# Optimization experiments

Measured on AMD Instinct MI355X. Metric: run time of the kernel, lower is better.

## Reference

```python
import jax, jax.numpy as jnp
import numpy as np
from jax import lax

PH = PW = 7  # patch size


def _unfold2d(x, ph, pw):
    # x: [B, C, H, W] -> patches [B*Ho*Wo, C*ph*pw], channel-major like F.unfold
    B, C, H, W = x.shape
    patches = lax.conv_general_dilated_patches(
        x, filter_shape=(ph, pw), window_strides=(1, 1), padding='VALID')
    # patches: [B, C*ph*pw, Ho, Wo] with feature order (c, i, j) matching F.unfold
    Ho, Wo = H - ph + 1, W - pw + 1
    D = C * ph * pw
    q2d = patches.reshape(B, D, Ho * Wo).transpose(0, 2, 1).reshape(B * Ho * Wo, D)
    return q2d, (B, C, H, W, Ho, Wo, D)


def _fold2d_mean(res, shape_info):
    # res: [B*Ho*Wo, D] patch values -> overlap-add mean image [B, C, H, W]
    B, C, H, W, Ho, Wo, D = shape_info
    res = res.reshape(B, Ho, Wo, C, PH, PW)
    out = jnp.zeros((B, C, H, W), dtype=res.dtype)
    cnt = jnp.zeros((H, W), dtype=res.dtype)
    for di in range(PH):          # small fixed 7x7 loop over patch offsets
        for dj in range(PW):
            out = out.at[:, :, di:di + Ho, dj:dj + Wo].add(
                res[:, :, :, :, di, dj].transpose(0, 3, 1, 2))
            cnt = cnt.at[di:di + Ho, dj:dj + Wo].add(1.0)
    return out / cnt  # reduce='mean'


def setup_inputs() -> dict:
    key = jax.random.key(0)
    k1, k2, k3 = jax.random.split(key, 3)
    query = jax.random.normal(k1, (1, 3, 96, 96), dtype=jnp.float32)
    kmat = jax.random.normal(k2, (8100, 147), dtype=jnp.float32)
    vmat = jax.random.normal(k3, (8100, 147), dtype=jnp.float32)
    return {"query": query, "key": kmat, "value": vmat}


def reference(query, key, value):
    # 1) unfold query image into patch rows [Nq, D]
    q2d, shape_info = _unfold2d(query, PH, PW)
    # 2) nearest-neighbor lookup: squared-euclidean argmin over key rows
    qn = jnp.sum(q2d * q2d, axis=1, keepdims=True)        # [Nq, 1]
    kn = jnp.sum(key * key, axis=1)                       # [Nk]
    dist = qn + kn[None, :] - 2.0 * (q2d @ key.T)         # [Nq, Nk]
    idx = jnp.argmin(dist, axis=1)                        # [Nq]
    # 3) gather matched value patches and fold back (overlap-add mean)
    res = value[idx]                                      # [Nq, D]
    return _fold2d_mean(res, shape_info)
```

## Files before the change

kernel.cpp:

```cpp
#include <hip/hip_runtime.h>


#define NQ 8100
#define NK 8100
#define DD 147
#define HO 90
#define IMG 96
#define NCH 5
#define CST 262144
#define ARRN (NCH * CST)

typedef _Float16 half8 __attribute__((ext_vector_type(8)));
typedef float f32x4 __attribute__((ext_vector_type(4)));

__device__ __forceinline__ void gld16(const _Float16* g, _Float16* l) {
    __builtin_amdgcn_global_load_lds(
        (const __attribute__((address_space(1))) unsigned int*)g,
        (__attribute__((address_space(3))) unsigned int*)l, 16, 0, 0);
}

__global__ void k_prep(const float* __restrict__ query, const float* __restrict__ key,
                       _Float16* __restrict__ Qh, _Float16* __restrict__ Ql,
                       _Float16* __restrict__ Kh, _Float16* __restrict__ Kl,
                       float* __restrict__ kn, unsigned long long* __restrict__ fidx64) {
    const int bx = blockIdx.x;
    const bool isK = (blockIdx.y != 0);

    if (bx >= 640) {
        if (!isK) return;
        int wave = threadIdx.x >> 6, lane = threadIdx.x & 63;
        int kb = ((bx - 640) * 4 + wave) * 16;
        for (int r = 0; r < 16; ++r) {
            int k = kb + r;
            float s = 0.f;
            if (k < NK)
                for (int d = lane; d < DD; d += 64) {
                    float v = key[k * DD + d];
                    s += v * v;
                }
#pragma unroll
            for (int off = 32; off; off >>= 1) s += __shfl_down(s, off, 64);
            if (lane == 0) {
                kn[k] = (k < NK) ? s : 1e30f;
                fidx64[k] = 0xFFFFFFFFFFFFFFFFull;
            }
        }
        return;
    }

    int t = bx * 256 + threadIdx.x;
    int c = t >> 15;
    int rem = t & 32767;
    int col = ((rem >> 6) << 4) + (rem & 15);
    int quad = (rem >> 4) & 3;
    int kbase = c * 32 + quad * 8;

    float v[8];
#pragma unroll
    for (int j = 0; j < 8; ++j) {
        int k = kbase + j;
        float x = 0.f;
        if (k < DD && col < NQ) {
            if (isK) {
                x = key[col * DD + k];
            } else {
                int c3 = k / 49, r2 = k - 49 * c3;
                int rr = r2 / 7, ss = r2 - 7 * rr;
                int y = col / HO, xx = col - HO * y;
                x = query[(c3 * IMG + y + rr) * IMG + xx + ss];
            }
        }
        v[j] = x;
    }
    half8 h8, l8;
#pragma unroll
    for (int j = 0; j < 8; ++j) {
        _Float16 h = (_Float16)v[j];
        h8[j] = h;
        l8[j] = (_Float16)((v[j] - (float)h) * 2048.0f);
    }
    if (isK) {
        *(half8*)(Kh + t * 8) = h8;
        *(half8*)(Kl + t * 8) = l8;
    } else {
        *(half8*)(Qh + t * 8) = h8;
        *(half8*)(Ql + t * 8) = l8;
    }
}

__launch_bounds__(256, 2)
__global__ void k_nn(const _Float16* __restrict__ Qh, const _Float16* __restrict__ Ql,
                     const _Float16* __restrict__ Kh, const _Float16* __restrict__ Kl,
                     const float* __restrict__ kn, unsigned long long* __restrict__ out) {
    __shared__ __align__(16) char smem[65536];
    _Float16* sbase = (_Float16*)smem;

    const int tid = (int)threadIdx.x;
    const int wave = tid >> 6, lane = tid & 63;
    const int l15 = lane & 15, quad = lane >> 4;

    const int b = (int)blockIdx.x;
    const int xcd = b & 7;
    const int i = b >> 3;
    const int qt = (xcd >> 1) * 16 + (i & 15);
    const int kt = (xcd & 1) * 32 + (i >> 4);

    const int mbase = (wave >> 1) * 64;
    const int nbase = (wave & 1) * 64;
    const int q0 = qt * 128, n0 = kt * 128;

    const _Float16* gsrc = (wave == 0) ? Qh : (wave == 1) ? Ql : (wave == 2) ? Kh : Kl;
    const int gbase = ((wave < 2) ? qt : kt) * 8;
    const _Float16* gp0 = gsrc + gbase * 512 + lane * 8;
    _Float16* ldst0 = sbase + wave * 4096 + lane * 8;

    f32x4 acc0[4][4], acc1[4][4];
#pragma unroll
    for (int ii = 0; ii < 4; ++ii)
#pragma unroll
        for (int j = 0; j < 4; ++j) {
            acc0[ii][j] = (f32x4)0.f;
            acc1[ii][j] = (f32x4)0.f;
        }

    const int agrp = (mbase >> 4);
    const int bgrp = (nbase >> 4);

#pragma unroll
    for (int grp = 0; grp < 8; ++grp)
        gld16(gp0 + grp * 512, ldst0 + grp * 512);

#pragma unroll
    for (int c = 0; c < NCH; ++c) {
        __syncthreads();
        if (c + 1 < NCH) {
            const _Float16* gp = gp0 + (c + 1) * CST;
            _Float16* ld = ldst0 + ((c + 1) & 1) * 16384;
#pragma unroll
            for (int grp = 0; grp < 8; ++grp)
                gld16(gp + grp * 512, ld + grp * 512);
        }

        const _Float16* sQh = sbase + (c & 1) * 16384;
        const _Float16* sQl = sQh + 4096;
        const _Float16* sKh = sQh + 8192;
        const _Float16* sKl = sQh + 12288;

        half8 ah[4], al[4];
#pragma unroll
        for (int mt = 0; mt < 4; ++mt) {
            int aoff = (agrp + mt) * 512 + lane * 8;
            ah[mt] = *(const half8*)(sQh + aoff);
            al[mt] = *(const half8*)(sQl + aoff);
        }
#pragma unroll
        for (int nt = 0; nt < 4; ++nt) {
            int boff = (bgrp + nt) * 512 + lane * 8;
            half8 bh = *(const half8*)(sKh + boff);
            half8 bl = *(const half8*)(sKl + boff);
#pragma unroll
            for (int mt = 0; mt < 4; ++mt) {
                acc0[mt][nt] = __builtin_amdgcn_mfma_f32_16x16x32_f16(ah[mt], bh, acc0[mt][nt], 0, 0, 0);
                acc1[mt][nt] = __builtin_amdgcn_mfma_f32_16x16x32_f16(ah[mt], bl, acc1[mt][nt], 0, 0, 0);
                acc1[mt][nt] = __builtin_amdgcn_mfma_f32_16x16x32_f16(al[mt], bh, acc1[mt][nt], 0, 0, 0);
            }
        }
    }

    float knv[4];
    int nglob[4];
#pragma unroll
    for (int nt = 0; nt < 4; ++nt) {
        nglob[nt] = n0 + nbase + nt * 16 + l15;
        knv[nt] = kn[nglob[nt]];
    }
    __syncthreads();
    float* redv = (float*)smem;
    int* redi = (int*)(smem + 17408);

#pragma unroll
    for (int mt = 0; mt < 4; ++mt)
#pragma unroll
        for (int r = 0; r < 4; ++r) {
            float bv = 1e38f;
            int bn = 0x7fffffff;
#pragma unroll
            for (int nt = 0; nt < 4; ++nt) {
                float d = knv[nt] - 2.0f * (acc0[mt][nt][r] + acc1[mt][nt][r] * (1.0f / 2048.0f));
                if (d < bv) { bv = d; bn = nglob[nt]; }
            }
            int m = mbase + mt * 16 + quad * 4 + r;
            int cidx = (nbase >> 2) + l15;
            redv[m * 33 + cidx] = bv;
            redi[m * 33 + cidx] = bn;
        }
    __syncthreads();

    if (tid < 128) {
        float bv = 1e38f;
        int bn = 0x7fffffff;
        for (int t2 = 0; t2 < 32; ++t2) {
            float v = redv[tid * 33 + t2];
            int n = redi[tid * 33 + t2];
            if (v < bv || (v == bv && n < bn)) { bv = v; bn = n; }
        }
        unsigned u = __float_as_uint(bv);
        u = (u & 0x80000000u) ? ~u : (u | 0x80000000u);
        unsigned long long pk = ((unsigned long long)u << 32) | (unsigned)bn;
        atomicMin(&out[q0 + tid], pk);
    }
}

__global__ void k_fold(const float* __restrict__ value,
                       const unsigned long long* __restrict__ fidx64,
                       float* __restrict__ out) {
    int t = blockIdx.x * 256 + threadIdx.x;
    if (t >= 3 * IMG * IMG) return;
    int c = t / (IMG * IMG);
    int rem = t % (IMG * IMG);
    int Y = rem / IMG, X = rem % IMG;
    int i0 = max(0, Y - (HO - 1)), i1 = min(6, Y);
    int j0 = max(0, X - (HO - 1)), j1 = min(6, X);
    float s = 0.f;
    for (int i = i0; i <= i1; ++i)
        for (int j = j0; j <= j1; ++j) {
            int p = (Y - i) * HO + (X - j);
            int row = (int)(fidx64[p] & 0xFFFFFFFFull);
            s += value[row * DD + c * 49 + i * 7 + j];
        }
    float cnt = (float)((i1 - i0 + 1) * (j1 - j0 + 1));
    out[t] = s / cnt;
}

extern "C" void kernel_launch(void* const* d_in, const int* in_sizes, int n_in,
                              void* d_out, int out_size, void* d_ws, size_t ws_size,
                              hipStream_t stream) {
    const float* query = (const float*)d_in[0];
    const float* key   = (const float*)d_in[1];
    const float* value = (const float*)d_in[2];
    float* out = (float*)d_out;

    _Float16* Qh = (_Float16*)d_ws;
    _Float16* Ql = Qh + ARRN;
    _Float16* Kh = Ql + ARRN;
    _Float16* Kl = Kh + ARRN;
    float* kn = (float*)(Kl + ARRN);
    unsigned long long* fidx64 = (unsigned long long*)(kn + 8192);

    dim3 gp(768, 2);
    k_prep<<<gp, 256, 0, stream>>>(query, key, Qh, Ql, Kh, Kl, kn, fidx64);
    k_nn<<<4096, 256, 0, stream>>>(Qh, Ql, Kh, Kl, kn, fidx64);
    k_fold<<<108, 256, 0, stream>>>(value, fidx64, out);
}
```

Before: 164.1 us.

## Keep query fragments in registers and loop over eight key tiles per block

The nearest-neighbour kernel now loads each block's query tile once into registers for all K-chunks. It then iterates over eight key tiles, reading key fragments straight from global memory instead of staging them through LDS with async loads. A running argmin is kept per query, so each block issues one atomicMin per query instead of one per key tile, and the grid shrinks from 4096 to 512 blocks. This trades LDS staging and double buffering for direct global loads and much higher register pressure (80 half8 query registers plus 32 accumulators), which may reduce occupancy. With 512 blocks there may also be too little parallelism to hide memory latency.

```diff
diff --git a/kernel.cpp b/kernel.cpp
--- a/kernel.cpp
+++ b/kernel.cpp
@@ -12,12 +12,6 @@
 
 typedef _Float16 half8 __attribute__((ext_vector_type(8)));
 typedef float f32x4 __attribute__((ext_vector_type(4)));
-
-__device__ __forceinline__ void gld16(const _Float16* g, _Float16* l) {
-    __builtin_amdgcn_global_load_lds(
-        (const __attribute__((address_space(1))) unsigned int*)g,
-        (__attribute__((address_space(3))) unsigned int*)l, 16, 0, 0);
-}
 
 __global__ void k_prep(const float* __restrict__ query, const float* __restrict__ key,
                        _Float16* __restrict__ Qh, _Float16* __restrict__ Ql,
@@ -92,121 +86,104 @@
 __global__ void k_nn(const _Float16* __restrict__ Qh, const _Float16* __restrict__ Ql,
                      const _Float16* __restrict__ Kh, const _Float16* __restrict__ Kl,
                      const float* __restrict__ kn, unsigned long long* __restrict__ out) {
-    __shared__ __align__(16) char smem[65536];
-    _Float16* sbase = (_Float16*)smem;
+    __shared__ float redv[128 * 33];
+    __shared__ int   redi[128 * 33];
 
     const int tid = (int)threadIdx.x;
     const int wave = tid >> 6, lane = tid & 63;
     const int l15 = lane & 15, quad = lane >> 4;
+    const int mbase = (wave >> 1) * 64;
+    const int nbase = (wave & 1) * 64;
 
     const int b = (int)blockIdx.x;
     const int xcd = b & 7;
-    const int i = b >> 3;
-    const int qt = (xcd >> 1) * 16 + (i & 15);
-    const int kt = (xcd & 1) * 32 + (i >> 4);
-
-    const int mbase = (wave >> 1) * 64;
-    const int nbase = (wave & 1) * 64;
-    const int q0 = qt * 128, n0 = kt * 128;
-
-    const _Float16* gsrc = (wave == 0) ? Qh : (wave == 1) ? Ql : (wave == 2) ? Kh : Kl;
-    const int gbase = ((wave < 2) ? qt : kt) * 8;
-    const _Float16* gp0 = gsrc + gbase * 512 + lane * 8;
-    _Float16* ldst0 = sbase + wave * 4096 + lane * 8;
-
-    f32x4 acc0[4][4], acc1[4][4];
-#pragma unroll
-    for (int ii = 0; ii < 4; ++ii)
-#pragma unroll
-        for (int j = 0; j < 4; ++j) {
-            acc0[ii][j] = (f32x4)0.f;
-            acc1[ii][j] = (f32x4)0.f;
-        }
-
-    const int agrp = (mbase >> 4);
-    const int bgrp = (nbase >> 4);
-
-#pragma unroll
-    for (int grp = 0; grp < 8; ++grp)
-        gld16(gp0 + grp * 512, ldst0 + grp * 512);
-
-#pragma unroll
-    for (int c = 0; c < NCH; ++c) {
+    const int j = b >> 3;
+    const int qt = (xcd >> 1) * 16 + (j & 15);
+    const int ktbase = (xcd & 1) * 32 + (j >> 4) * 8;
+    const int q0 = qt * 128;
+
+    half8 qh[NCH][4], ql[NCH][4];
+#pragma unroll
+    for (int c = 0; c < NCH; ++c)
+#pragma unroll
+        for (int mt = 0; mt < 4; ++mt) {
+            int off = c * CST + (qt * 8 + (mbase >> 4) + mt) * 512 + lane * 8;
+            qh[c][mt] = *(const half8*)(Qh + off);
+            ql[c][mt] = *(const half8*)(Ql + off);
+        }
+
+    float rbv = 1e38f;
+    int rbn = 0x7fffffff;
+
+    for (int t = 0; t < 8; ++t) {
+        const int kts = ktbase + t;
+        f32x4 acc0[4][4], acc1[4][4];
+#pragma unroll
+        for (int i = 0; i < 4; ++i)
+#pragma unroll
+            for (int jj = 0; jj < 4; ++jj) {
+                acc0[i][jj] = (f32x4)0.f;
+                acc1[i][jj] = (f32x4)0.f;
+            }
+
+        const int kgrp = (kts * 8 + (nbase >> 4)) * 512 + lane * 8;
+#pragma unroll
+        for (int c = 0; c < NCH; ++c) {
+            half8 bh[4], bl[4];
+#pragma unroll
+            for (int nt = 0; nt < 4; ++nt) {
+                bh[nt] = *(const half8*)(Kh + c * CST + kgrp + nt * 512);
+                bl[nt] = *(const half8*)(Kl + c * CST + kgrp + nt * 512);
+            }
+#pragma unroll
+            for (int nt = 0; nt < 4; ++nt)
+#pragma unroll
+                for (int mt = 0; mt < 4; ++mt) {
+                    acc0[mt][nt] = __builtin_amdgcn_mfma_f32_16x16x32_f16(qh[c][mt], bh[nt], acc0[mt][nt], 0, 0, 0);
+                    acc1[mt][nt] = __builtin_amdgcn_mfma_f32_16x16x32_f16(qh[c][mt], bl[nt], acc1[mt][nt], 0, 0, 0);
+                    acc1[mt][nt] = __builtin_amdgcn_mfma_f32_16x16x32_f16(ql[c][mt], bh[nt], acc1[mt][nt], 0, 0, 0);
+                }
+        }
+
+        float knv[4];
+        int nglob[4];
+#pragma unroll
+        for (int nt = 0; nt < 4; ++nt) {
+            nglob[nt] = kts * 128 + nbase + nt * 16 + l15;
+            knv[nt] = kn[nglob[nt]];
+        }
         __syncthreads();
-        if (c + 1 < NCH) {
-            const _Float16* gp = gp0 + (c + 1) * CST;
-            _Float16* ld = ldst0 + ((c + 1) & 1) * 16384;
-#pragma unroll
-            for (int grp = 0; grp < 8; ++grp)
-                gld16(gp + grp * 512, ld + grp * 512);
-        }
-
-        const _Float16* sQh = sbase + (c & 1) * 16384;
-        const _Float16* sQl = sQh + 4096;
-        const _Float16* sKh = sQh + 8192;
-        const _Float16* sKl = sQh + 12288;
-
-        half8 ah[4], al[4];
-#pragma unroll
-        for (int mt = 0; mt < 4; ++mt) {
-            int aoff = (agrp + mt) * 512 + lane * 8;
-            ah[mt] = *(const half8*)(sQh + aoff);
-            al[mt] = *(const half8*)(sQl + aoff);
-        }
-#pragma unroll
-        for (int nt = 0; nt < 4; ++nt) {
-            int boff = (bgrp + nt) * 512 + lane * 8;
-            half8 bh = *(const half8*)(sKh + boff);
-            half8 bl = *(const half8*)(sKl + boff);
-#pragma unroll
-            for (int mt = 0; mt < 4; ++mt) {
-                acc0[mt][nt] = __builtin_amdgcn_mfma_f32_16x16x32_f16(ah[mt], bh, acc0[mt][nt], 0, 0, 0);
-                acc1[mt][nt] = __builtin_amdgcn_mfma_f32_16x16x32_f16(ah[mt], bl, acc1[mt][nt], 0, 0, 0);
-                acc1[mt][nt] = __builtin_amdgcn_mfma_f32_16x16x32_f16(al[mt], bh, acc1[mt][nt], 0, 0, 0);
-            }
-        }
-    }
-
-    float knv[4];
-    int nglob[4];
-#pragma unroll
-    for (int nt = 0; nt < 4; ++nt) {
-        nglob[nt] = n0 + nbase + nt * 16 + l15;
-        knv[nt] = kn[nglob[nt]];
-    }
-    __syncthreads();
-    float* redv = (float*)smem;
-    int* redi = (int*)(smem + 17408);
-
-#pragma unroll
-    for (int mt = 0; mt < 4; ++mt)
-#pragma unroll
-        for (int r = 0; r < 4; ++r) {
-            float bv = 1e38f;
-            int bn = 0x7fffffff;
-#pragma unroll
-            for (int nt = 0; nt < 4; ++nt) {
-                float d = knv[nt] - 2.0f * (acc0[mt][nt][r] + acc1[mt][nt][r] * (1.0f / 2048.0f));
-                if (d < bv) { bv = d; bn = nglob[nt]; }
-            }
-            int m = mbase + mt * 16 + quad * 4 + r;
-            int cidx = (nbase >> 2) + l15;
-            redv[m * 33 + cidx] = bv;
-            redi[m * 33 + cidx] = bn;
-        }
-    __syncthreads();
+#pragma unroll
+        for (int mt = 0; mt < 4; ++mt)
+#pragma unroll
+            for (int r = 0; r < 4; ++r) {
+                float bv = 1e38f;
+                int bn = 0x7fffffff;
+#pragma unroll
+                for (int nt = 0; nt < 4; ++nt) {
+                    float d = knv[nt] - 2.0f * (acc0[mt][nt][r] + acc1[mt][nt][r] * (1.0f / 2048.0f));
+                    if (d < bv) { bv = d; bn = nglob[nt]; }
+                }
+                int m = mbase + mt * 16 + quad * 4 + r;
+                int cidx = (nbase >> 2) + l15;
+                redv[m * 33 + cidx] = bv;
+                redi[m * 33 + cidx] = bn;
+            }
+        __syncthreads();
+
+        if (tid < 128) {
+            for (int t2 = 0; t2 < 32; ++t2) {
+                float v = redv[tid * 33 + t2];
+                int n = redi[tid * 33 + t2];
+                if (v < rbv || (v == rbv && n < rbn)) { rbv = v; rbn = n; }
+            }
+        }
+    }
 
     if (tid < 128) {
-        float bv = 1e38f;
-        int bn = 0x7fffffff;
-        for (int t2 = 0; t2 < 32; ++t2) {
-            float v = redv[tid * 33 + t2];
-            int n = redi[tid * 33 + t2];
-            if (v < bv || (v == bv && n < bn)) { bv = v; bn = n; }
-        }
-        unsigned u = __float_as_uint(bv);
+        unsigned u = __float_as_uint(rbv);
         u = (u & 0x80000000u) ? ~u : (u | 0x80000000u);
-        unsigned long long pk = ((unsigned long long)u << 32) | (unsigned)bn;
+        unsigned long long pk = ((unsigned long long)u << 32) | (unsigned)rbn;
         atomicMin(&out[q0 + tid], pk);
     }
 }
@@ -249,6 +226,6 @@
 
     dim3 gp(768, 2);
     k_prep<<<gp, 256, 0, stream>>>(query, key, Qh, Ql, Kh, Kl, kn, fidx64);
-    k_nn<<<4096, 256, 0, stream>>>(Qh, Ql, Kh, Kl, kn, fidx64);
+    k_nn<<<512, 256, 0, stream>>>(Qh, Ql, Kh, Kl, kn, fidx64);
     k_fold<<<108, 256, 0, stream>>>(value, fidx64, out);
 }
```

New measurement: 239.8 us. +46.1%, slower.

## Keep query tile resident in LDS and loop eight key tiles per block

Applied to the files above, without the earlier changes.

Each k_nn block now loads its whole 128-row query tile (high and low halves, all five K-chunks) into LDS once, then iterates over eight key tiles. Key fragments are read straight from global memory instead of being staged through LDS. The running argmin stays in registers across key tiles and is reduced with cross-lane shuffles, which shrinks the shared-memory reduction buffers. The grid drops from 4096 to 512 blocks. This cuts redundant query loads and atomics, but uses 80KB of LDS per block, which may limit occupancy to one block per CU. Key loads are also no longer prefetched, which may expose global-memory latency to the MFMA loop.

```diff
diff --git a/kernel.cpp b/kernel.cpp
--- a/kernel.cpp
+++ b/kernel.cpp
@@ -92,121 +92,127 @@
 __global__ void k_nn(const _Float16* __restrict__ Qh, const _Float16* __restrict__ Ql,
                      const _Float16* __restrict__ Kh, const _Float16* __restrict__ Kl,
                      const float* __restrict__ kn, unsigned long long* __restrict__ out) {
-    __shared__ __align__(16) char smem[65536];
-    _Float16* sbase = (_Float16*)smem;
+    __shared__ __align__(16) char smem[81920];
+    _Float16* sQh = (_Float16*)smem;
+    _Float16* sQl = (_Float16*)(smem + 40960);
 
     const int tid = (int)threadIdx.x;
     const int wave = tid >> 6, lane = tid & 63;
     const int l15 = lane & 15, quad = lane >> 4;
+    const int mbase = (wave >> 1) * 64;
+    const int nbase = (wave & 1) * 64;
 
     const int b = (int)blockIdx.x;
     const int xcd = b & 7;
     const int i = b >> 3;
     const int qt = (xcd >> 1) * 16 + (i & 15);
-    const int kt = (xcd & 1) * 32 + (i >> 4);
-
-    const int mbase = (wave >> 1) * 64;
-    const int nbase = (wave & 1) * 64;
-    const int q0 = qt * 128, n0 = kt * 128;
-
-    const _Float16* gsrc = (wave == 0) ? Qh : (wave == 1) ? Ql : (wave == 2) ? Kh : Kl;
-    const int gbase = ((wave < 2) ? qt : kt) * 8;
-    const _Float16* gp0 = gsrc + gbase * 512 + lane * 8;
-    _Float16* ldst0 = sbase + wave * 4096 + lane * 8;
-
-    f32x4 acc0[4][4], acc1[4][4];
-#pragma unroll
-    for (int ii = 0; ii < 4; ++ii)
-#pragma unroll
-        for (int j = 0; j < 4; ++j) {
-            acc0[ii][j] = (f32x4)0.f;
-            acc1[ii][j] = (f32x4)0.f;
-        }
+    const int ktbase = ((xcd & 1) * 4 + (i >> 4)) * 8;
+    const int q0 = qt * 128;
+
+    {
+        const _Float16* gq = (const _Float16*)(lane * 8);
+#pragma unroll
+        for (int s = 0; s < 20; ++s) {
+            int seg = s * 4 + wave;
+            int a = seg / 40, rem = seg % 40;
+            int c = rem >> 3, g = rem & 7;
+            const _Float16* gp = (a ? Ql : Qh) + c * CST + (qt * 8 + g) * 512 + lane * 8;
+            _Float16* ld = (_Float16*)smem + a * 20480 + (c * 8 + g) * 512 + lane * 8;
+            gld16(gp, ld);
+        }
+        (void)gq;
+    }
+    __syncthreads();
+
+    float rbv[16];
+    int rbn[16];
+#pragma unroll
+    for (int r = 0; r < 16; ++r) { rbv[r] = 1e38f; rbn[r] = 0x7fffffff; }
 
     const int agrp = (mbase >> 4);
     const int bgrp = (nbase >> 4);
 
-#pragma unroll
-    for (int grp = 0; grp < 8; ++grp)
-        gld16(gp0 + grp * 512, ldst0 + grp * 512);
-
-#pragma unroll
-    for (int c = 0; c < NCH; ++c) {
-        __syncthreads();
-        if (c + 1 < NCH) {
-            const _Float16* gp = gp0 + (c + 1) * CST;
-            _Float16* ld = ldst0 + ((c + 1) & 1) * 16384;
-#pragma unroll
-            for (int grp = 0; grp < 8; ++grp)
-                gld16(gp + grp * 512, ld + grp * 512);
-        }
-
-        const _Float16* sQh = sbase + (c & 1) * 16384;
-        const _Float16* sQl = sQh + 4096;
-        const _Float16* sKh = sQh + 8192;
-        const _Float16* sKl = sQh + 12288;
-
-        half8 ah[4], al[4];
-#pragma unroll
-        for (int mt = 0; mt < 4; ++mt) {
-            int aoff = (agrp + mt) * 512 + lane * 8;
-            ah[mt] = *(const half8*)(sQh + aoff);
-            al[mt] = *(const half8*)(sQl + aoff);
-        }
+    for (int t = 0; t < 8; ++t) {
+        const int kts = ktbase + t;
+        f32x4 acc0[4][4], acc1[4][4];
+#pragma unroll
+        for (int ii = 0; ii < 4; ++ii)
+#pragma unroll
+            for (int jj = 0; jj < 4; ++jj) {
+                acc0[ii][jj] = (f32x4)0.f;
+                acc1[ii][jj] = (f32x4)0.f;
+            }
+
+        const int kgoff = (kts * 8 + bgrp) * 512 + lane * 8;
+#pragma unroll
+        for (int c = 0; c < NCH; ++c) {
+            half8 ah[4], al[4];
+#pragma unroll
+            for (int mt = 0; mt < 4; ++mt) {
+                int aoff = c * 4096 + (agrp + mt) * 512 + lane * 8;
+                ah[mt] = *(const half8*)(sQh + aoff);
+                al[mt] = *(const half8*)(sQl + aoff);
+            }
+#pragma unroll
+            for (int nt = 0; nt < 4; ++nt) {
+                half8 bh = *(const half8*)(Kh + c * CST + kgoff + nt * 512);
+                half8 bl = *(const half8*)(Kl + c * CST + kgoff + nt * 512);
+#pragma unroll
+                for (int mt = 0; mt < 4; ++mt) {
+                    acc0[mt][nt] = __builtin_amdgcn_mfma_f32_16x16x32_f16(ah[mt], bh, acc0[mt][nt], 0, 0, 0);
+                    acc1[mt][nt] = __builtin_amdgcn_mfma_f32_16x16x32_f16(ah[mt], bl, acc1[mt][nt], 0, 0, 0);
+                    acc1[mt][nt] = __builtin_amdgcn_mfma_f32_16x16x32_f16(al[mt], bh, acc1[mt][nt], 0, 0, 0);
+                }
+            }
+        }
+
 #pragma unroll
         for (int nt = 0; nt < 4; ++nt) {
-            int boff = (bgrp + nt) * 512 + lane * 8;
-            half8 bh = *(const half8*)(sKh + boff);
-            half8 bl = *(const half8*)(sKl + boff);
-#pragma unroll
-            for (int mt = 0; mt < 4; ++mt) {
-                acc0[mt][nt] = __builtin_amdgcn_mfma_f32_16x16x32_f16(ah[mt], bh, acc0[mt][nt], 0, 0, 0);
-                acc1[mt][nt] = __builtin_amdgcn_mfma_f32_16x16x32_f16(ah[mt], bl, acc1[mt][nt], 0, 0, 0);
-                acc1[mt][nt] = __builtin_amdgcn_mfma_f32_16x16x32_f16(al[mt], bh, acc1[mt][nt], 0, 0, 0);
-            }
-        }
-    }
-
-    float knv[4];
-    int nglob[4];
-#pragma unroll
-    for (int nt = 0; nt < 4; ++nt) {
-        nglob[nt] = n0 + nbase + nt * 16 + l15;
-        knv[nt] = kn[nglob[nt]];
-    }
+            int n = kts * 128 + nbase + nt * 16 + l15;
+            float knv = kn[n];
+#pragma unroll
+            for (int mt = 0; mt < 4; ++mt)
+#pragma unroll
+                for (int r = 0; r < 4; ++r) {
+                    float d = knv - 2.0f * (acc0[mt][nt][r] + acc1[mt][nt][r] * (1.0f / 2048.0f));
+                    int ri = mt * 4 + r;
+                    if (d < rbv[ri]) { rbv[ri] = d; rbn[ri] = n; }
+                }
+        }
+    }
+
+#pragma unroll
+    for (int ri = 0; ri < 16; ++ri) {
+#pragma unroll
+        for (int m = 1; m < 16; m <<= 1) {
+            float vo = __shfl_xor(rbv[ri], m, 64);
+            int no = __shfl_xor(rbn[ri], m, 64);
+            if (vo < rbv[ri] || (vo == rbv[ri] && no < rbn[ri])) { rbv[ri] = vo; rbn[ri] = no; }
+        }
+    }
+
     __syncthreads();
     float* redv = (float*)smem;
-    int* redi = (int*)(smem + 17408);
-
-#pragma unroll
-    for (int mt = 0; mt < 4; ++mt)
-#pragma unroll
-        for (int r = 0; r < 4; ++r) {
-            float bv = 1e38f;
-            int bn = 0x7fffffff;
-#pragma unroll
-            for (int nt = 0; nt < 4; ++nt) {
-                float d = knv[nt] - 2.0f * (acc0[mt][nt][r] + acc1[mt][nt][r] * (1.0f / 2048.0f));
-                if (d < bv) { bv = d; bn = nglob[nt]; }
-            }
-            int m = mbase + mt * 16 + quad * 4 + r;
-            int cidx = (nbase >> 2) + l15;
-            redv[m * 33 + cidx] = bv;
-            redi[m * 33 + cidx] = bn;
-        }
+    int* redi = (int*)(smem + 1024);
+    if (l15 == 0) {
+#pragma unroll
+        for (int mt = 0; mt < 4; ++mt)
+#pragma unroll
+            for (int r = 0; r < 4; ++r) {
+                int m = mbase + mt * 16 + quad * 4 + r;
+                redv[m * 2 + (wave & 1)] = rbv[mt * 4 + r];
+                redi[m * 2 + (wave & 1)] = rbn[mt * 4 + r];
+            }
+    }
     __syncthreads();
 
     if (tid < 128) {
-        float bv = 1e38f;
-        int bn = 0x7fffffff;
-        for (int t2 = 0; t2 < 32; ++t2) {
-            float v = redv[tid * 33 + t2];
-            int n = redi[tid * 33 + t2];
-            if (v < bv || (v == bv && n < bn)) { bv = v; bn = n; }
-        }
-        unsigned u = __float_as_uint(bv);
+        float v0 = redv[tid * 2], v1 = redv[tid * 2 + 1];
+        int n0 = redi[tid * 2], n1 = redi[tid * 2 + 1];
+        if (v1 < v0 || (v1 == v0 && n1 < n0)) { v0 = v1; n0 = n1; }
+        unsigned u = __float_as_uint(v0);
         u = (u & 0x80000000u) ? ~u : (u | 0x80000000u);
-        unsigned long long pk = ((unsigned long long)u << 32) | (unsigned)bn;
+        unsigned long long pk = ((unsigned long long)u << 32) | (unsigned)n0;
         atomicMin(&out[q0 + tid], pk);
     }
 }
@@ -249,6 +255,6 @@
 
     dim3 gp(768, 2);
     k_prep<<<gp, 256, 0, stream>>>(query, key, Qh, Ql, Kh, Kl, kn, fidx64);
-    k_nn<<<4096, 256, 0, stream>>>(Qh, Ql, Kh, Kl, kn, fidx64);
+    k_nn<<<512, 256, 0, stream>>>(Qh, Ql, Kh, Kl, kn, fidx64);
     k_fold<<<108, 256, 0, stream>>>(value, fidx64, out);
 }
```

New measurement: 241.8 us. +47.3%, slower.
